# Kernel tuning notes

Measured on AMD Instinct MI355X. Metric: run time of the kernel, lower is better.

Reference implementation:

```python
import jax, jax.numpy as jnp
import numpy as np


def group_norm(x, g, b, groups, eps=1e-5):
    # x: (B, C, H, W), PyTorch GroupNorm semantics
    B, C, H, W = x.shape
    xr = x.reshape(B, groups, -1)
    m = xr.mean(-1, keepdims=True)
    v = xr.var(-1, keepdims=True)
    xn = ((xr - m) * jax.lax.rsqrt(v + eps)).reshape(B, C, H, W)
    return xn * g[:, None, None] + b[:, None, None]


def mamba(xs, in_w, conv_w, conv_b, xproj_w, dt_w, dt_b, A_log, D, out_w):
    # Standard Mamba block: in_proj -> causal depthwise conv -> SiLU ->
    # x_proj -> softplus(dt_proj) -> selective scan -> gate -> out_proj.
    Bsz, L, d = xs.shape
    di = in_w.shape[0] // 2
    r = dt_w.shape[1]
    n = A_log.shape[1]
    K = conv_w.shape[1]
    xz = xs @ in_w.T                           # (B, L, 2*di)
    xpart, z = xz[..., :di], xz[..., di:]
    xp = jnp.pad(xpart, ((0, 0), (K - 1, 0), (0, 0)))  # causal pad
    xc = conv_b + sum(xp[:, k:k + L, :] * conv_w[:, k] for k in range(K))
    xc = jax.nn.silu(xc)
    proj = xc @ xproj_w.T                      # (B, L, r + 2n)
    dt = proj[..., :r]
    Bm = proj[..., r:r + n]
    Cm = proj[..., r + n:]
    delta = jax.nn.softplus(dt @ dt_w.T + dt_b)   # (B, L, di)
    A = -jnp.exp(A_log)                            # (di, n)
    dA = jnp.exp(jnp.einsum('bld,dn->bldn', delta, A))
    dBu = jnp.einsum('bld,bln,bld->bldn', delta, Bm, xc)

    def step(h, inp):
        dA_t, dBu_t, C_t = inp
        h = dA_t * h + dBu_t                  # (B, di, n)
        return h, jnp.einsum('bdn,bn->bd', h, C_t)

    h0 = jnp.zeros((Bsz, di, n), xs.dtype)
    _, ys = jax.lax.scan(step, h0, (jnp.moveaxis(dA, 1, 0), jnp.moveaxis(dBu, 1, 0), jnp.moveaxis(Cm, 1, 0)))
    y = jnp.moveaxis(ys, 0, 1) + D * xc
    y = y * jax.nn.silu(z)
    return y @ out_w.T


def setup_inputs() -> dict:
    def nrm(i, shape, s=0.05):
        return jax.random.normal(jax.random.fold_in(jax.random.key(0), i), shape, dtype=jnp.float32) * s

    f32 = jnp.float32
    C = 128
    di, r, n = 256, 8, 16          # spa mamba: d_model=128, expand=2
    di2, r2 = 64, 2                # spe mamba: d_model=32
    A1 = jnp.log(jnp.broadcast_to(jnp.arange(1, n + 1, dtype=f32), (di, n)))
    A2 = jnp.log(jnp.broadcast_to(jnp.arange(1, n + 1, dtype=f32), (di2, n)))
    return {
        'x': nrm(0, (2, C, 64, 64), 1.0),
        'pe_w': nrm(1, (C, C)), 'pe_b': jnp.zeros((C,), f32),
        'pe_gn_g': jnp.ones((C,), f32), 'pe_gn_b': jnp.zeros((C,), f32),
        'spa_in_w': nrm(2, (2 * di, C)),
        'spa_conv_w': nrm(3, (di, 4)), 'spa_conv_b': jnp.zeros((di,), f32),
        'spa_xproj_w': nrm(4, (r + 2 * n, di)),
        'spa_dt_w': nrm(5, (di, r)), 'spa_dt_b': jnp.full((di,), -2.0, f32),
        'spa_Alog': A1, 'spa_D': jnp.ones((di,), f32),
        'spa_out_w': nrm(6, (C, di)),
        'spa_gn_g': jnp.ones((C,), f32), 'spa_gn_b': jnp.zeros((C,), f32),
        'spe_in_w': nrm(7, (2 * di2, 32)),
        'spe_conv_w': nrm(8, (di2, 4)), 'spe_conv_b': jnp.zeros((di2,), f32),
        'spe_xproj_w': nrm(9, (r2 + 2 * n, di2)),
        'spe_dt_w': nrm(10, (di2, r2)), 'spe_dt_b': jnp.full((di2,), -2.0, f32),
        'spe_Alog': A2, 'spe_D': jnp.ones((di2,), f32),
        'spe_out_w': nrm(11, (32, di2)),
        'spe_gn_g': jnp.ones((C,), f32), 'spe_gn_b': jnp.zeros((C,), f32),
        'fuse_w': jnp.full((2,), 0.5, f32),
        'cls_w': nrm(12, (10, C)), 'cls_b': jnp.zeros((10,), f32),
        'ref_dw_w': nrm(13, (C, 1, 3, 3)),
        'ref_gn_g': jnp.ones((C,), f32), 'ref_gn_b': jnp.zeros((C,), f32),
        'ref_pw_w': nrm(14, (1, C)), 'ref_pw_b': jnp.zeros((1,), f32),
        'alpha': jnp.asarray(1e-4, f32),
    }


def reference(x, pe_w, pe_b, pe_gn_g, pe_gn_b, spa_in_w, spa_conv_w, spa_conv_b, spa_xproj_w, spa_dt_w, spa_dt_b, spa_Alog, spa_D, spa_out_w, spa_gn_g, spa_gn_b, spe_in_w, spe_conv_w, spe_conv_b, spe_xproj_w, spe_dt_w, spe_dt_b, spe_Alog, spe_D, spe_out_w, spe_gn_g, spe_gn_b, fuse_w, cls_w, cls_b, ref_dw_w, ref_gn_g, ref_gn_b, ref_pw_w, ref_pw_b, alpha):
    B, _, H, W = x.shape
    # patch embedding: 1x1 conv + GroupNorm + SiLU
    h1 = jnp.einsum('bchw,oc->bohw', x, pe_w) + pe_b[:, None, None]
    h1 = jax.nn.silu(group_norm(h1, pe_gn_g, pe_gn_b, 4))
    # SpaMamba: scan over flattened spatial tokens (B, H*W, C)
    seq = h1.transpose(0, 2, 3, 1).reshape(B, H * W, -1)
    y = mamba(seq, spa_in_w, spa_conv_w, spa_conv_b, spa_xproj_w, spa_dt_w, spa_dt_b, spa_Alog, spa_D, spa_out_w)
    y = y.reshape(B, H, W, -1).transpose(0, 3, 1, 2)
    spa = jax.nn.silu(group_norm(y, spa_gn_g, spa_gn_b, 4)) + h1
    # SpeMamba: token_num=4, group_channel_num=32, channel_num=128 (no pad)
    seq2 = h1.transpose(0, 2, 3, 1).reshape(B * H * W, 4, 32)
    y2 = mamba(seq2, spe_in_w, spe_conv_w, spe_conv_b, spe_xproj_w, spe_dt_w, spe_dt_b, spe_Alog, spe_D, spe_out_w)
    y2 = y2.reshape(B, H, W, -1).transpose(0, 3, 1, 2)
    spe = h1 + jax.nn.silu(group_norm(y2, spe_gn_g, spe_gn_b, 4))
    # attention-weighted fusion + residual (BothMamba, use_att=True)
    wts = jax.nn.softmax(fuse_w)
    feat = spa * wts[0] + spe * wts[1] + h1
    # classifier head (1x1 conv)
    logits = jnp.einsum('bchw,oc->bohw', feat, cls_w) + cls_b[:, None, None]
    # BoundaryAwareLogitRefiner
    edge = jax.lax.conv_general_dilated(feat, ref_dw_w, (1, 1), ((1, 1), (1, 1)), feature_group_count=feat.shape[1], dimension_numbers=('NCHW', 'OIHW', 'NCHW'))
    edge = jax.nn.silu(group_norm(edge, ref_gn_g, ref_gn_b, 4))
    edge = jax.nn.sigmoid(jnp.einsum('bchw,oc->bohw', edge, ref_pw_w) + ref_pw_b[:, None, None])
    local = jax.lax.reduce_window(logits, 0.0, jax.lax.add, (1, 1, 3, 3), (1, 1, 1, 1), ((0, 0), (0, 0), (1, 1), (1, 1))) / 9.0  # count_include_pad=True
    return logits + alpha * (1.0 - edge) * (local - logits)
```

## Files before the change

### kernel.cpp

```cpp
#include <hip/hip_runtime.h>
#include <math.h>

#define DEV __device__ __forceinline__

DEV float sigm(float x){ return 1.f/(1.f+__expf(-x)); }
DEV float siluf(float x){ return x * sigm(x); }
DEV float softplusf(float x){ return x > 20.f ? x : log1pf(__expf(x)); }

static constexpr float NG = 131072.0f;
static constexpr float LOG2E = 1.4426950408889634f;

static constexpr size_t WS_H1    = 0;
static constexpr size_t WS_H1PRE = 1048576;
static constexpr size_t WS_XC    = 2097152;
static constexpr size_t WS_ZSIL  = 4194304;
static constexpr size_t WS_XZD   = 6291456;
static constexpr size_t WS_QOFF  = 8388608;
static constexpr size_t WS_LOG   = 8650752;
static constexpr size_t WS_Y     = 10485760;
static constexpr size_t WS_POFF  = 12582912;
static constexpr size_t WS_Y2    = 14155776;
static constexpr size_t WS_PROJ  = 15204352;

DEV void reduce_part(const float* __restrict__ part, int rowsPerB, float* dst16){
  int tid = threadIdx.x;
  int p = tid >> 4, sl = tid & 15;
  int b = p >> 3, j = p & 7;
  float s = 0.f;
  for (int row = sl; row < rowsPerB; row += 16)
    s += part[((size_t)b*rowsPerB + row)*8 + j];
  s += __shfl_xor(s,1); s += __shfl_xor(s,2);
  s += __shfl_xor(s,4); s += __shfl_xor(s,8);
  if (sl == 0) dst16[p] = s;
  __syncthreads();
}

__global__ void __launch_bounds__(256)
k_pe(const float* __restrict__ x, const float* __restrict__ pe_w,
     const float* __restrict__ pe_b, float* __restrict__ h1pre,
     float* __restrict__ part){
  __shared__ float As[16][36];
  __shared__ float Bs[16][64];
  __shared__ float red1[2][4], red2[2][4];
  int tid = threadIdx.x;
  int nx = blockIdx.x, my = blockIdx.y;
  int m0 = my*32, n0 = nx*64;
  int b = m0 >> 12, pl0 = m0 & 4095;
  int tx = tid & 15, ty = tid >> 4;
  float acc[2][4];
  #pragma unroll
  for (int i = 0; i < 2; i++)
    #pragma unroll
    for (int j = 0; j < 4; j++) acc[i][j] = 0.f;
  for (int k0 = 0; k0 < 128; k0 += 16){
    if (tid < 128){
      int k = tid >> 3, mm = (tid & 7)*4;
      float4 a = *(const float4*)(x + ((size_t)b*128 + k0+k)*4096 + pl0 + mm);
      *(float4*)&As[k][mm] = a;
    }
    {
      int n = tid >> 2, kq = (tid & 3)*4;
      float4 a = *(const float4*)(pe_w + (size_t)(n0+n)*128 + k0 + kq);
      Bs[kq+0][n] = a.x; Bs[kq+1][n] = a.y; Bs[kq+2][n] = a.z; Bs[kq+3][n] = a.w;
    }
    __syncthreads();
    #pragma unroll
    for (int k = 0; k < 16; k++){
      float2 av = *(const float2*)&As[k][ty*2];
      float4 bv = *(const float4*)&Bs[k][tx*4];
      acc[0][0] += av.x*bv.x; acc[0][1] += av.x*bv.y; acc[0][2] += av.x*bv.z; acc[0][3] += av.x*bv.w;
      acc[1][0] += av.y*bv.x; acc[1][1] += av.y*bv.y; acc[1][2] += av.y*bv.z; acc[1][3] += av.y*bv.w;
    }
    __syncthreads();
  }
  float4 bias = *(const float4*)(pe_b + n0 + tx*4);
  float s1 = 0.f, s2 = 0.f;
  #pragma unroll
  for (int i = 0; i < 2; i++){
    float4 st;
    st.x = acc[i][0]+bias.x; st.y = acc[i][1]+bias.y;
    st.z = acc[i][2]+bias.z; st.w = acc[i][3]+bias.w;
    s1 += st.x+st.y+st.z+st.w;
    s2 += st.x*st.x + st.y*st.y + st.z*st.z + st.w*st.w;
    *(float4*)(h1pre + (size_t)(m0 + ty*2 + i)*128 + n0 + tx*4) = st;
  }
  s1 += __shfl_xor(s1,1);  s2 += __shfl_xor(s2,1);
  s1 += __shfl_xor(s1,2);  s2 += __shfl_xor(s2,2);
  s1 += __shfl_xor(s1,4);  s2 += __shfl_xor(s2,4);
  s1 += __shfl_xor(s1,16); s2 += __shfl_xor(s2,16);
  s1 += __shfl_xor(s1,32); s2 += __shfl_xor(s2,32);
  int lane = tid & 63, w = tid >> 6;
  if ((lane & 55) == 0){
    int gl = (lane >> 3) & 1;
    red1[gl][w] = s1; red2[gl][w] = s2;
  }
  __syncthreads();
  if (tid < 8){
    int gg = tid >> 1, which = tid & 1;
    int gl = gg - nx*2;
    float v = 0.f;
    if (gl == 0 || gl == 1){
      v = which ? (red2[gl][0]+red2[gl][1]+red2[gl][2]+red2[gl][3])
                : (red1[gl][0]+red1[gl][1]+red1[gl][2]+red1[gl][3]);
    }
    int pblk = b*256 + (my & 127)*2 + nx;
    part[(size_t)pblk*8 + tid] = v;
  }
}

__global__ void __launch_bounds__(256)
k_xz(const float* __restrict__ h1pre, const float* __restrict__ in_w,
     const float* __restrict__ partPE, const float* __restrict__ gng,
     const float* __restrict__ gnb, float* __restrict__ h1,
     float* __restrict__ xzd, float* __restrict__ zsil){
  __shared__ float As[16][68];
  __shared__ float Bs[16][64];
  __shared__ float sst[16];
  reduce_part(partPE, 256, sst);
  int tid = threadIdx.x;
  int m0 = blockIdx.y*64, n0 = blockIdx.x*64;
  int tx = tid & 15, ty = tid >> 4;
  float acc[4][4];
  #pragma unroll
  for (int i = 0; i < 4; i++)
    #pragma unroll
    for (int j = 0; j < 4; j++) acc[i][j] = 0.f;
  for (int k0 = 0; k0 < 128; k0 += 16){
    {
      int m = tid >> 2, kk = (tid & 3)*4;
      int pixm = m0 + m, c0 = k0 + kk;
      int bb = pixm >> 12, g = c0 >> 5;
      float4 a = *(const float4*)(h1pre + (size_t)pixm*128 + c0);
      float mu = sst[bb*8 + g*2] * (1.f/NG);
      float var = sst[bb*8 + g*2 + 1] * (1.f/NG) - mu*mu;
      float rs = rsqrtf(var + 1e-5f);
      float4 gg = *(const float4*)(gng + c0);
      float4 gb = *(const float4*)(gnb + c0);
      float4 v;
      v.x = siluf((a.x-mu)*rs*gg.x + gb.x);
      v.y = siluf((a.y-mu)*rs*gg.y + gb.y);
      v.z = siluf((a.z-mu)*rs*gg.z + gb.z);
      v.w = siluf((a.w-mu)*rs*gg.w + gb.w);
      As[kk+0][m] = v.x; As[kk+1][m] = v.y; As[kk+2][m] = v.z; As[kk+3][m] = v.w;
      if (blockIdx.x == 0) *(float4*)(h1 + (size_t)pixm*128 + c0) = v;
    }
    {
      int n = tid >> 2, kq = (tid & 3)*4;
      float4 a = *(const float4*)(in_w + (size_t)(n0+n)*128 + k0 + kq);
      Bs[kq+0][n] = a.x; Bs[kq+1][n] = a.y; Bs[kq+2][n] = a.z; Bs[kq+3][n] = a.w;
    }
    __syncthreads();
    #pragma unroll
    for (int k = 0; k < 16; k++){
      float4 av = *(const float4*)&As[k][ty*4];
      float4 bv = *(const float4*)&Bs[k][tx*4];
      acc[0][0] += av.x*bv.x; acc[0][1] += av.x*bv.y; acc[0][2] += av.x*bv.z; acc[0][3] += av.x*bv.w;
      acc[1][0] += av.y*bv.x; acc[1][1] += av.y*bv.y; acc[1][2] += av.y*bv.z; acc[1][3] += av.y*bv.w;
      acc[2][0] += av.z*bv.x; acc[2][1] += av.z*bv.y; acc[2][2] += av.z*bv.z; acc[2][3] += av.z*bv.w;
      acc[3][0] += av.w*bv.x; acc[3][1] += av.w*bv.y; acc[3][2] += av.w*bv.z; acc[3][3] += av.w*bv.w;
    }
    __syncthreads();
  }
  if (n0 < 256){
    #pragma unroll
    for (int i = 0; i < 4; i++){
      float4 st; st.x = acc[i][0]; st.y = acc[i][1]; st.z = acc[i][2]; st.w = acc[i][3];
      *(float4*)(xzd + (size_t)(m0 + ty*4 + i)*256 + n0 + tx*4) = st;
    }
  } else {
    #pragma unroll
    for (int i = 0; i < 4; i++){
      float4 st;
      st.x = siluf(acc[i][0]); st.y = siluf(acc[i][1]);
      st.z = siluf(acc[i][2]); st.w = siluf(acc[i][3]);
      *(float4*)(zsil + (size_t)(m0 + ty*4 + i)*256 + (n0-256) + tx*4) = st;
    }
  }
}

__global__ void __launch_bounds__(256)
k_projc(const float* __restrict__ xzd, const float* __restrict__ cw,
        const float* __restrict__ cb, const float* __restrict__ xpw,
        const float* __restrict__ dtw, const float* __restrict__ dtb,
        const float* __restrict__ Alog,
        float* __restrict__ xc, float* __restrict__ proj,
        float* __restrict__ delta, float* __restrict__ P,
        float* __restrict__ Q){
  __shared__ float xct[16*260];
  __shared__ float s_pr[16][40];
  int tid = threadIdx.x;
  int bc = blockIdx.x;
  int m0 = bc * 16;
  {
    int slot = tid >> 6, lane = tid & 63;
    int d4 = lane*4;
    float4 cbv = *(const float4*)(cb + d4);
    float4 cw0 = *(const float4*)(cw + (size_t)(d4+0)*4);
    float4 cw1 = *(const float4*)(cw + (size_t)(d4+1)*4);
    float4 cw2 = *(const float4*)(cw + (size_t)(d4+2)*4);
    float4 cw3 = *(const float4*)(cw + (size_t)(d4+3)*4);
    const float* c0p = (const float*)&cw0;
    const float* c1p = (const float*)&cw1;
    const float* c2p = (const float*)&cw2;
    const float* c3p = (const float*)&cw3;
    for (int i = 0; i < 4; i++){
      int t = slot*4 + i;
      int tok = m0 + t;
      int l = tok & 4095;
      float4 acc = cbv;
      #pragma unroll
      for (int k = 0; k < 4; k++){
        int ls = l - 3 + k;
        if (ls >= 0){
          float4 xv = *(const float4*)(xzd + (size_t)(tok-3+k)*256 + d4);
          acc.x += xv.x * c0p[k];
          acc.y += xv.y * c1p[k];
          acc.z += xv.z * c2p[k];
          acc.w += xv.w * c3p[k];
        }
      }
      float4 s;
      s.x = siluf(acc.x); s.y = siluf(acc.y); s.z = siluf(acc.z); s.w = siluf(acc.w);
      *(float4*)&xct[t*260 + d4] = s;
      *(float4*)(xc + (size_t)tok*256 + d4) = s;
    }
  }
  __syncthreads();
  {
    int t = tid & 15, jq = tid >> 4;
    int tok = m0 + t;
    float a0 = 0.f, a1 = 0.f, a2 = 0.f;
    for (int k0 = 0; k0 < 256; k0 += 4){
      float4 av = *(const float4*)&xct[t*260 + k0];
      float4 w0 = *(const float4*)(xpw + (size_t)jq*256 + k0);
      float4 w1 = *(const float4*)(xpw + (size_t)(jq+16)*256 + k0);
      a0 += av.x*w0.x + av.y*w0.y + av.z*w0.z + av.w*w0.w;
      a1 += av.x*w1.x + av.y*w1.y + av.z*w1.z + av.w*w1.w;
      if (jq < 8){
        float4 w2 = *(const float4*)(xpw + (size_t)(jq+32)*256 + k0);
        a2 += av.x*w2.x + av.y*w2.y + av.z*w2.z + av.w*w2.w;
      }
    }
    float* pr = proj + (size_t)tok*40;
    pr[jq] = a0;      s_pr[t][jq] = a0;
    pr[jq+16] = a1;   s_pr[t][jq+16] = a1;
    if (jq < 8){ pr[jq+32] = a2; s_pr[t][jq+32] = a2; }
  }
  __syncthreads();
  {
    int d = tid;
    const float4* wr = (const float4*)(dtw + (size_t)d*8);
    float4 w0 = wr[0], w1 = wr[1];
    float bd = dtb[d];
    float An[16];
    {
      const float4* ar = (const float4*)(Alog + (size_t)d*16);
      #pragma unroll
      for (int k = 0; k < 4; k++){
        float4 a = ar[k];
        An[k*4]   = -__expf(a.x)*LOG2E; An[k*4+1] = -__expf(a.y)*LOG2E;
        An[k*4+2] = -__expf(a.z)*LOG2E; An[k*4+3] = -__expf(a.w)*LOG2E;
      }
    }
    float Pv[16], Qv[16];
    #pragma unroll
    for (int n = 0; n < 16; n++){ Pv[n] = 1.f; Qv[n] = 0.f; }
    for (int t = 0; t < 16; t++){
      float dv = bd + s_pr[t][0]*w0.x + s_pr[t][1]*w0.y + s_pr[t][2]*w0.z + s_pr[t][3]*w0.w
                    + s_pr[t][4]*w1.x + s_pr[t][5]*w1.y + s_pr[t][6]*w1.z + s_pr[t][7]*w1.w;
      dv = softplusf(dv);
      delta[(size_t)(m0+t)*256 + d] = dv;
      float xv = xct[t*260 + d];
      float dBx = dv*xv;
      #pragma unroll
      for (int n = 0; n < 16; n++){
        float a = exp2f(dv*An[n]);
        Qv[n] = a*Qv[n] + s_pr[t][8+n]*dBx;
        Pv[n] *= a;
      }
    }
    float* Pp = P + (size_t)bc*4096 + d*16;
    float* Qp = Q + (size_t)bc*4096 + d*16;
    #pragma unroll
    for (int k = 0; k < 4; k++){
      float4 pv; pv.x=Pv[k*4]; pv.y=Pv[k*4+1]; pv.z=Pv[k*4+2]; pv.w=Pv[k*4+3];
      float4 qv; qv.x=Qv[k*4]; qv.y=Qv[k*4+1]; qv.z=Qv[k*4+2]; qv.w=Qv[k*4+3];
      *(float4*)(Pp + k*4) = pv;
      *(float4*)(Qp + k*4) = qv;
    }
  }
}

__global__ void __launch_bounds__(256)
k_scan2(const float* __restrict__ P, const float* __restrict__ Q,
        float* __restrict__ hs){
  __shared__ float Ps[256][17], Qs[256][17];
  int tid = threadIdx.x;
  int b = blockIdx.x >> 8;
  int dn0 = (blockIdx.x & 255) * 16;
  for (int i = tid; i < 1024; i += 256){
    int ch = i >> 2, g = (i & 3)*4;
    size_t gaddr = (size_t)(b*256+ch)*4096 + dn0 + g;
    float4 p = *(const float4*)(P + gaddr);
    float4 q = *(const float4*)(Q + gaddr);
    Ps[ch][g]=p.x; Ps[ch][g+1]=p.y; Ps[ch][g+2]=p.z; Ps[ch][g+3]=p.w;
    Qs[ch][g]=q.x; Qs[ch][g+1]=q.y; Qs[ch][g+2]=q.z; Qs[ch][g+3]=q.w;
  }
  __syncthreads();
  int lane = tid & 63, wv = tid >> 6;
  for (int rep = 0; rep < 4; rep++){
    int c = wv*4 + rep;
    float p0 = Ps[4*lane+0][c], q0 = Qs[4*lane+0][c];
    float p1 = Ps[4*lane+1][c], q1 = Qs[4*lane+1][c];
    float p2 = Ps[4*lane+2][c], q2 = Qs[4*lane+2][c];
    float p3 = Ps[4*lane+3][c], q3 = Qs[4*lane+3][c];
    float p = p0, q = q0;
    q = p1*q + q1; p *= p1;
    q = p2*q + q2; p *= p2;
    q = p3*q + q3; p *= p3;
    #pragma unroll
    for (int off = 1; off < 64; off <<= 1){
      float pp = __shfl_up(p, off);
      float qp = __shfl_up(q, off);
      if (lane >= off){ q = p*qp + q; p = p*pp; }
    }
    float h0 = __shfl_up(q, 1);
    if (lane == 0) h0 = 0.f;
    float h1 = p0*h0 + q0;
    float h2 = p1*h1 + q1;
    float h3 = p2*h2 + q2;
    Ps[4*lane+0][c] = h0;
    Ps[4*lane+1][c] = h1;
    Ps[4*lane+2][c] = h2;
    Ps[4*lane+3][c] = h3;
  }
  __syncthreads();
  for (int i = tid; i < 1024; i += 256){
    int ch = i >> 2, g = (i & 3)*4;
    size_t gaddr = (size_t)(b*256+ch)*4096 + dn0 + g;
    float4 h;
    h.x = Ps[ch][g]; h.y = Ps[ch][g+1]; h.z = Ps[ch][g+2]; h.w = Ps[ch][g+3];
    *(float4*)(hs + gaddr) = h;
  }
}

__global__ void __launch_bounds__(256)
k_scan3(const float* __restrict__ delta, const float* __restrict__ proj,
        const float* __restrict__ xc, const float* __restrict__ zsil,
        const float* __restrict__ Alog, const float* __restrict__ Dv,
        const float* __restrict__ hs, float* __restrict__ y){
  int blk = blockIdx.x;
  int dblk = blk & 3;
  int bc = blk >> 2;
  int b = bc >> 8, chunk = bc & 255;
  int tid = threadIdx.x;
  int dl = tid >> 2, ng = tid & 3;
  int d = dblk*64 + dl;
  float4 a4 = *(const float4*)(Alog + (size_t)d*16 + ng*4);
  float An[4] = {-__expf(a4.x)*LOG2E, -__expf(a4.y)*LOG2E,
                 -__expf(a4.z)*LOG2E, -__expf(a4.w)*LOG2E};
  float Dd = Dv[d];
  float h[4];
  {
    size_t o = (size_t)bc*4096 + dblk*1024 + tid*4;
    float4 hv = *(const float4*)(hs + o);
    h[0]=hv.x; h[1]=hv.y; h[2]=hv.z; h[3]=hv.w;
  }
  size_t row0 = (size_t)(b*4096 + chunk*16);
  for (int l = 0; l < 16; l++){
    size_t r = row0 + l;
    float dv = delta[r*256 + d];
    float xv = xc[r*256 + d];
    float4 bm = *(const float4*)(proj + r*40 + 8 + ng*4);
    float4 cm = *(const float4*)(proj + r*40 + 24 + ng*4);
    float dBx = dv*xv;
    float bmv[4] = {bm.x, bm.y, bm.z, bm.w};
    float cmv[4] = {cm.x, cm.y, cm.z, cm.w};
    float ys = 0.f;
    #pragma unroll
    for (int k = 0; k < 4; k++){
      float a = exp2f(dv*An[k]);
      h[k] = a*h[k] + bmv[k]*dBx;
      ys += h[k]*cmv[k];
    }
    ys += __shfl_xor(ys, 1);
    ys += __shfl_xor(ys, 2);
    if (ng == 0){
      float zv = zsil[r*256 + d];
      y[r*256 + d] = (ys + Dd*xv) * zv;
    }
  }
}

__global__ void __launch_bounds__(256)
k_outproj(const float* __restrict__ y, const float* __restrict__ out_w,
          float* __restrict__ yproj, float* __restrict__ part){
  __shared__ float As[16][36];
  __shared__ float Bs[16][64];
  __shared__ float red1[2][4], red2[2][4];
  int tid = threadIdx.x;
  int nx = blockIdx.x, my = blockIdx.y;
  int m0 = my*32, n0 = nx*64;
  int b = m0 >> 12;
  int tx = tid & 15, ty = tid >> 4;
  float acc[2][4];
  #pragma unroll
  for (int i = 0; i < 2; i++)
    #pragma unroll
    for (int j = 0; j < 4; j++) acc[i][j] = 0.f;
  for (int k0 = 0; k0 < 256; k0 += 16){
    if (tid < 128){
      int m = tid >> 2, kk = (tid & 3)*4;
      float4 a = *(const float4*)(y + (size_t)(m0+m)*256 + k0+kk);
      As[kk+0][m] = a.x; As[kk+1][m] = a.y; As[kk+2][m] = a.z; As[kk+3][m] = a.w;
    }
    {
      int n = tid >> 2, kq = (tid & 3)*4;
      float4 a = *(const float4*)(out_w + (size_t)(n0+n)*256 + k0 + kq);
      Bs[kq+0][n] = a.x; Bs[kq+1][n] = a.y; Bs[kq+2][n] = a.z; Bs[kq+3][n] = a.w;
    }
    __syncthreads();
    #pragma unroll
    for (int k = 0; k < 16; k++){
      float2 av = *(const float2*)&As[k][ty*2];
      float4 bv = *(const float4*)&Bs[k][tx*4];
      acc[0][0] += av.x*bv.x; acc[0][1] += av.x*bv.y; acc[0][2] += av.x*bv.z; acc[0][3] += av.x*bv.w;
      acc[1][0] += av.y*bv.x; acc[1][1] += av.y*bv.y; acc[1][2] += av.y*bv.z; acc[1][3] += av.y*bv.w;
    }
    __syncthreads();
  }
  float s1 = 0.f, s2 = 0.f;
  #pragma unroll
  for (int i = 0; i < 2; i++){
    float4 st; st.x = acc[i][0]; st.y = acc[i][1]; st.z = acc[i][2]; st.w = acc[i][3];
    s1 += st.x+st.y+st.z+st.w;
    s2 += st.x*st.x + st.y*st.y + st.z*st.z + st.w*st.w;
    *(float4*)(yproj + (size_t)(m0 + ty*2 + i)*128 + n0 + tx*4) = st;
  }
  s1 += __shfl_xor(s1,1);  s2 += __shfl_xor(s2,1);
  s1 += __shfl_xor(s1,2);  s2 += __shfl_xor(s2,2);
  s1 += __shfl_xor(s1,4);  s2 += __shfl_xor(s2,4);
  s1 += __shfl_xor(s1,16); s2 += __shfl_xor(s2,16);
  s1 += __shfl_xor(s1,32); s2 += __shfl_xor(s2,32);
  int lane = tid & 63, w = tid >> 6;
  if ((lane & 55) == 0){
    int gl = (lane >> 3) & 1;
    red1[gl][w] = s1; red2[gl][w] = s2;
  }
  __syncthreads();
  if (tid < 8){
    int gg = tid >> 1, which = tid & 1;
    int gl = gg - nx*2;
    float v = 0.f;
    if (gl == 0 || gl == 1){
      v = which ? (red2[gl][0]+red2[gl][1]+red2[gl][2]+red2[gl][3])
                : (red1[gl][0]+red1[gl][1]+red1[gl][2]+red1[gl][3]);
    }
    int pblk = b*256 + (my & 127)*2 + nx;
    part[(size_t)pblk*8 + tid] = v;
  }
}

__global__ void __launch_bounds__(256)
k_spe_ab(const float* __restrict__ h1, const float* __restrict__ in_w,
         const float* __restrict__ conv_w, const float* __restrict__ conv_b,
         const float* __restrict__ xpw, float* __restrict__ xc2,
         float* __restrict__ zsil2, float* __restrict__ proj2){
  __shared__ float s_in[4][128];
  __shared__ float s_xc[64][66];
  int tid = threadIdx.x;
  int w = tid >> 6, lane = tid & 63;
  {
    float wx[32], wz[32];
    const float4* rx = (const float4*)(in_w + (size_t)lane*32);
    const float4* rz = (const float4*)(in_w + (size_t)(64+lane)*32);
    #pragma unroll
    for (int k = 0; k < 8; k++){
      float4 a = rx[k]; wx[k*4]=a.x; wx[k*4+1]=a.y; wx[k*4+2]=a.z; wx[k*4+3]=a.w;
      float4 b = rz[k]; wz[k*4]=b.x; wz[k*4+1]=b.y; wz[k*4+2]=b.z; wz[k*4+3]=b.w;
    }
    float4 cwv = ((const float4*)conv_w)[lane];
    float cbv = conv_b[lane];
    for (int i = 0; i < 4; i++){
      int pix = blockIdx.x*16 + w*4 + i;
      float2 hv = ((const float2*)(h1 + (size_t)pix*128))[lane];
      s_in[w][2*lane] = hv.x; s_in[w][2*lane+1] = hv.y;
      float xpr[4], zs[4];
      #pragma unroll
      for (int l = 0; l < 4; l++){
        const float4* sv = (const float4*)&s_in[w][l*32];
        float ax = 0.f, az = 0.f;
        #pragma unroll
        for (int c4 = 0; c4 < 8; c4++){
          float4 v = sv[c4];
          ax += v.x*wx[c4*4] + v.y*wx[c4*4+1] + v.z*wx[c4*4+2] + v.w*wx[c4*4+3];
          az += v.x*wz[c4*4] + v.y*wz[c4*4+1] + v.z*wz[c4*4+2] + v.w*wz[c4*4+3];
        }
        xpr[l] = ax; zs[l] = siluf(az);
      }
      #pragma unroll
      for (int l = 0; l < 4; l++){
        float v = cbv;
        if (l >= 3) v += xpr[l-3]*cwv.x;
        if (l >= 2) v += xpr[l-2]*cwv.y;
        if (l >= 1) v += xpr[l-1]*cwv.z;
        v += xpr[l]*cwv.w;
        float sx = siluf(v);
        int t = (w*4+i)*4 + l;
        int tok = blockIdx.x*64 + t;
        s_xc[t][lane] = sx;
        xc2 [(size_t)tok*64 + lane] = sx;
        zsil2[(size_t)tok*64 + lane] = zs[l];
      }
    }
  }
  __syncthreads();
  {
    int t = lane;
    float a[9];
    #pragma unroll
    for (int j = 0; j < 9; j++) a[j] = 0.f;
    for (int k = 0; k < 64; k++){
      float xk = s_xc[t][k];
      #pragma unroll
      for (int j = 0; j < 9; j++){
        int ja = w*9 + j; if (ja > 33) ja = 33;
        a[j] += xk * xpw[(size_t)ja*64 + k];
      }
    }
    float* pr = proj2 + (size_t)(blockIdx.x*64 + t)*36;
    #pragma unroll
    for (int j = 0; j < 9; j++){
      int ja = w*9 + j;
      if (ja < 34) pr[ja] = a[j];
    }
  }
}

__global__ void __launch_bounds__(256)
k_spe_cd(const float* __restrict__ xc2, const float* __restrict__ zsil2,
         const float* __restrict__ proj, const float* __restrict__ dt_w,
         const float* __restrict__ dt_b, const float* __restrict__ Alog,
         const float* __restrict__ Dvec, const float* __restrict__ out_w,
         float* __restrict__ y2, float* __restrict__ part){
  __shared__ float s_y[64][68];
  __shared__ float ldsWT[64*32];
  __shared__ float bst[8];
  int tid = threadIdx.x;
  int w = tid >> 6, lane = tid & 63;
  for (int i = tid; i < 2048; i += 256){
    int c2 = i >> 6, dd = i & 63;
    ldsWT[dd*32 + c2] = out_w[i];
  }
  if (tid < 8) bst[tid] = 0.f;
  {
    float2 dtwv = ((const float2*)dt_w)[lane];
    float dbv = dt_b[lane], Dd = Dvec[lane];
    float An[16];
    const float4* ar = (const float4*)(Alog + (size_t)lane*16);
    #pragma unroll
    for (int k = 0; k < 4; k++){
      float4 a = ar[k];
      An[k*4]   = -__expf(a.x)*LOG2E; An[k*4+1] = -__expf(a.y)*LOG2E;
      An[k*4+2] = -__expf(a.z)*LOG2E; An[k*4+3] = -__expf(a.w)*LOG2E;
    }
    for (int i = 0; i < 4; i++){
      int pix = blockIdx.x*16 + w*4 + i;
      float h[16];
      #pragma unroll
      for (int n = 0; n < 16; n++) h[n] = 0.f;
      #pragma unroll
      for (int l = 0; l < 4; l++){
        int tok = pix*4 + l;
        float pj[36];
        {
          const float4* pr = (const float4*)(proj + (size_t)tok*36);
          #pragma unroll
          for (int k = 0; k < 9; k++){
            float4 v = pr[k];
            pj[k*4]=v.x; pj[k*4+1]=v.y; pj[k*4+2]=v.z; pj[k*4+3]=v.w;
          }
        }
        float xv = xc2[(size_t)tok*64 + lane];
        float zv = zsil2[(size_t)tok*64 + lane];
        float dt = softplusf(dbv + pj[0]*dtwv.x + pj[1]*dtwv.y);
        float ys = 0.f;
        #pragma unroll
        for (int n = 0; n < 16; n++){
          float a = exp2f(dt * An[n]);
          h[n] = a*h[n] + dt * pj[2+n] * xv;
          ys += h[n] * pj[18+n];
        }
        s_y[(w*4+i)*4 + l][lane] = (ys + Dd*xv) * zv;
      }
    }
  }
  __syncthreads();
  {
    int c2 = lane & 31, slot = lane >> 5;
    int tl0 = w*16 + slot;
    float acc[8];
    #pragma unroll
    for (int i = 0; i < 8; i++) acc[i] = 0.f;
    for (int dd4 = 0; dd4 < 16; dd4++){
      float w0 = ldsWT[(dd4*4+0)*32 + c2];
      float w1 = ldsWT[(dd4*4+1)*32 + c2];
      float w2 = ldsWT[(dd4*4+2)*32 + c2];
      float w3 = ldsWT[(dd4*4+3)*32 + c2];
      #pragma unroll
      for (int i = 0; i < 8; i++){
        int t = tl0 + 2*i;
        float4 yv = *(const float4*)&s_y[t][dd4*4];
        acc[i] += yv.x*w0 + yv.y*w1 + yv.z*w2 + yv.w*w3;
      }
    }
    #pragma unroll
    for (int i = 0; i < 8; i++){
      int tok = blockIdx.x*64 + tl0 + 2*i;
      int pix = tok >> 2, l = tok & 3;
      y2[(size_t)pix*128 + l*32 + c2] = acc[i];
      float s1 = acc[i], s2 = acc[i]*acc[i];
      s1 += __shfl_xor(s1,1);  s2 += __shfl_xor(s2,1);
      s1 += __shfl_xor(s1,2);  s2 += __shfl_xor(s2,2);
      s1 += __shfl_xor(s1,4);  s2 += __shfl_xor(s2,4);
      s1 += __shfl_xor(s1,8);  s2 += __shfl_xor(s2,8);
      s1 += __shfl_xor(s1,16); s2 += __shfl_xor(s2,16);
      if (c2 == 0){
        atomicAdd(&bst[l*2+0], s1);
        atomicAdd(&bst[l*2+1], s2);
      }
    }
  }
  __syncthreads();
  if (tid < 8) part[(size_t)blockIdx.x*8 + tid] = bst[tid];
}

__global__ void __launch_bounds__(256)
k_fusedw(const float* __restrict__ h1, const float* __restrict__ yproj,
         const float* __restrict__ y2, const float* __restrict__ partSPA,
         const float* __restrict__ partSPE,
         const float* __restrict__ spa_g, const float* __restrict__ spa_b,
         const float* __restrict__ spe_g, const float* __restrict__ spe_b,
         const float* __restrict__ fuse_w, const float* __restrict__ cls_w,
         const float* __restrict__ cls_b, const float* __restrict__ dww,
         float* __restrict__ logits, float* __restrict__ epre,
         float* __restrict__ part){
  __shared__ float ft[60*129];
  __shared__ float clsL[10*129];
  __shared__ float sst[32];
  __shared__ float red1[4][64], red2[4][64];
  int tid = threadIdx.x;
  reduce_part(partSPA, 256, sst);
  reduce_part(partSPE, 256, sst+16);
  for (int i = tid; i < 1280; i += 256){
    int o = i >> 7, cc = i & 127;
    clsL[o*129 + cc] = cls_w[o*128 + cc];
  }
  int blk = blockIdx.x;
  int b = blk >> 7, rem = blk & 127;
  int ty = rem >> 3, tx = rem & 7;
  int r0 = ty*4, c0 = tx*8;
  float e0 = __expf(fuse_w[0]), e1 = __expf(fuse_w[1]);
  float wA = e0/(e0+e1), wB = e1/(e0+e1);
  for (int idx = tid; idx < 7680; idx += 256){
    int pos = idx >> 7, c = idx & 127;
    int hr = pos/10, hc = pos - hr*10;
    int ry = r0 + hr - 1, rx = c0 + hc - 1;
    float f = 0.f;
    if (ry >= 0 && ry < 64 && rx >= 0 && rx < 64){
      size_t pix = (size_t)((b<<12)|(ry<<6)|rx);
      int g = c >> 5;
      float m1 = sst[b*8 + g*2]      * (1.f/NG);
      float v1 = sst[b*8 + g*2 + 1]  * (1.f/NG) - m1*m1;
      float m2 = sst[16 + b*8 + g*2] * (1.f/NG);
      float v2 = sst[16 + b*8 + g*2+1]*(1.f/NG) - m2*m2;
      float h = h1[pix*128 + c];
      float sa = siluf((yproj[pix*128+c]-m1)*rsqrtf(v1+1e-5f)*spa_g[c] + spa_b[c]) + h;
      float sp = h + siluf((y2[pix*128+c]-m2)*rsqrtf(v2+1e-5f)*spe_g[c] + spe_b[c]);
      f = sa*wA + sp*wB + h;
    }
    ft[pos*129 + c] = f;
  }
  __syncthreads();
  int c = tid & 127, pl = tid >> 7;
  float w9[9];
  #pragma unroll
  for (int k = 0; k < 9; k++) w9[k] = dww[c*9+k];
  float s1 = 0.f, s2 = 0.f;
  for (int i = 0; i < 16; i++){
    int px = i*2 + pl;
    int py = px >> 3, pxx = px & 7;
    float acc = 0.f;
    #pragma unroll
    for (int dy = 0; dy < 3; dy++)
      #pragma unroll
      for (int dx = 0; dx < 3; dx++)
        acc += ft[((py+dy)*10 + (pxx+dx))*129 + c] * w9[dy*3+dx];
    epre[(size_t)((b<<12)|((r0+py)<<6)|(c0+pxx))*128 + c] = acc;
    s1 += acc; s2 += acc*acc;
  }
  for (int idx = tid; idx < 320; idx += 256){
    int px = idx/10, o = idx - px*10;
    int py = px >> 3, pxx = px & 7;
    int pos = (py+1)*10 + (pxx+1);
    float acc = cls_b[o];
    for (int cc = 0; cc < 128; cc++)
      acc += ft[pos*129 + cc] * clsL[o*129 + cc];
    logits[(size_t)((b<<12)|((r0+py)<<6)|(c0+pxx))*16 + o] = acc;
  }
  int g = c >> 5;
  int ridx0 = (c & 31) | (pl << 5);
  red1[g][ridx0] = s1; red2[g][ridx0] = s2;
  __syncthreads();
  int rg = tid >> 6, ridx = tid & 63;
  for (int s = 32; s >= 1; s >>= 1){
    if (ridx < s){ red1[rg][ridx] += red1[rg][ridx+s]; red2[rg][ridx] += red2[rg][ridx+s]; }
    __syncthreads();
  }
  if (ridx == 0){
    part[(size_t)blk*8 + rg*2+0] = red1[rg][0];
    part[(size_t)blk*8 + rg*2+1] = red2[rg][0];
  }
}

__global__ void __launch_bounds__(256)
k_final(const float* __restrict__ epre, const float* __restrict__ logits,
        const float* __restrict__ partDW, const float* __restrict__ rg_g,
        const float* __restrict__ rg_b, const float* __restrict__ pw_w,
        const float* __restrict__ pw_b, const float* __restrict__ alpha,
        float* __restrict__ outp){
  __shared__ float sst[16];
  __shared__ float part[4];
  __shared__ float edge_s[2];
  reduce_part(partDW, 128, sst);
  int tid = threadIdx.x;
  int pixl = tid >> 7, c = tid & 127;
  int pix = blockIdx.x*2 + pixl;
  int b = pix >> 12, p = pix & 4095, yy = p >> 6, xx = p & 63;
  int g = c >> 5;
  float m = sst[b*8 + g*2]   * (1.f/NG);
  float v = sst[b*8 + g*2+1] * (1.f/NG) - m*m;
  float e = epre[(size_t)pix*128+c];
  float en = siluf((e-m)*rsqrtf(v+1e-5f)*rg_g[c] + rg_b[c]);
  float pv = en * pw_w[c];
  pv += __shfl_xor(pv,1);  pv += __shfl_xor(pv,2);  pv += __shfl_xor(pv,4);
  pv += __shfl_xor(pv,8);  pv += __shfl_xor(pv,16); pv += __shfl_xor(pv,32);
  if ((tid & 63) == 0) part[tid>>6] = pv;
  __syncthreads();
  if (tid < 2) edge_s[tid] = sigm(part[tid*2] + part[tid*2+1] + pw_b[0]);
  __syncthreads();
  if (c < 10){
    float ed = edge_s[pixl];
    int o = c;
    float lg = logits[(size_t)pix*16 + o];
    float loc = 0.f;
    for (int dy = -1; dy <= 1; dy++){
      int ny = yy+dy; if (ny < 0 || ny > 63) continue;
      for (int dx = -1; dx <= 1; dx++){
        int nx = xx+dx; if (nx < 0 || nx > 63) continue;
        loc += logits[(size_t)((b<<12)|(ny<<6)|nx)*16 + o];
      }
    }
    loc *= (1.f/9.f);
    outp[(size_t)((b*10+o)<<12) + p] = lg + alpha[0]*(1.f-ed)*(loc - lg);
  }
}

extern "C" void kernel_launch(void* const* d_in, const int* in_sizes, int n_in,
                              void* d_out, int out_size, void* d_ws, size_t ws_size,
                              hipStream_t stream){
  const float* x          = (const float*)d_in[0];
  const float* pe_w       = (const float*)d_in[1];
  const float* pe_b       = (const float*)d_in[2];
  const float* pe_gn_g    = (const float*)d_in[3];
  const float* pe_gn_b    = (const float*)d_in[4];
  const float* spa_in_w   = (const float*)d_in[5];
  const float* spa_conv_w = (const float*)d_in[6];
  const float* spa_conv_b = (const float*)d_in[7];
  const float* spa_xproj_w= (const float*)d_in[8];
  const float* spa_dt_w   = (const float*)d_in[9];
  const float* spa_dt_b   = (const float*)d_in[10];
  const float* spa_Alog   = (const float*)d_in[11];
  const float* spa_D      = (const float*)d_in[12];
  const float* spa_out_w  = (const float*)d_in[13];
  const float* spa_gn_g   = (const float*)d_in[14];
  const float* spa_gn_b   = (const float*)d_in[15];
  const float* spe_in_w   = (const float*)d_in[16];
  const float* spe_conv_w = (const float*)d_in[17];
  const float* spe_conv_b = (const float*)d_in[18];
  const float* spe_xproj_w= (const float*)d_in[19];
  const float* spe_dt_w   = (const float*)d_in[20];
  const float* spe_dt_b   = (const float*)d_in[21];
  const float* spe_Alog   = (const float*)d_in[22];
  const float* spe_D      = (const float*)d_in[23];
  const float* spe_out_w  = (const float*)d_in[24];
  const float* spe_gn_g   = (const float*)d_in[25];
  const float* spe_gn_b   = (const float*)d_in[26];
  const float* fuse_w     = (const float*)d_in[27];
  const float* cls_w      = (const float*)d_in[28];
  const float* cls_b      = (const float*)d_in[29];
  const float* ref_dw_w   = (const float*)d_in[30];
  const float* ref_gn_g   = (const float*)d_in[31];
  const float* ref_gn_b   = (const float*)d_in[32];
  const float* ref_pw_w   = (const float*)d_in[33];
  const float* ref_pw_b   = (const float*)d_in[34];
  const float* alpha      = (const float*)d_in[35];
  float* ws  = (float*)d_ws;
  float* out = (float*)d_out;

  float* Pb    = ws + WS_POFF;
  float* Qb    = ws + WS_QOFF;
  float* HSb   = Pb;
  float* dely  = ws + WS_Y;
  float* partPE  = ws + WS_Y;
  float* partSPA = ws + WS_POFF;
  float* partSPE = ws + WS_POFF + 16384;
  float* partDW  = ws + WS_POFF + 65536;
  float* proj  = ws + WS_PROJ;
  float* xc2   = ws + WS_XC;
  float* zsil2 = ws + WS_XZD;
  float* proj2 = ws + WS_QOFF;
  float* epre  = ws + WS_Y;

  k_pe<<<dim3(2,256),256,0,stream>>>(x, pe_w, pe_b, ws+WS_H1PRE, partPE);
  k_xz<<<dim3(8,128),256,0,stream>>>(ws+WS_H1PRE, spa_in_w, partPE,
      pe_gn_g, pe_gn_b, ws+WS_H1, ws+WS_XZD, ws+WS_ZSIL);
  k_projc<<<512,256,0,stream>>>(ws+WS_XZD, spa_conv_w, spa_conv_b, spa_xproj_w,
      spa_dt_w, spa_dt_b, spa_Alog, ws+WS_XC, proj, dely, Pb, Qb);
  k_scan2<<<512,256,0,stream>>>(Pb, Qb, HSb);
  k_scan3<<<2048,256,0,stream>>>(dely, proj, ws+WS_XC, ws+WS_ZSIL,
      spa_Alog, spa_D, HSb, dely);
  k_outproj<<<dim3(2,256),256,0,stream>>>(dely, spa_out_w, ws+WS_H1PRE, partSPA);
  k_spe_ab<<<512,256,0,stream>>>(ws+WS_H1, spe_in_w, spe_conv_w, spe_conv_b,
      spe_xproj_w, xc2, zsil2, proj2);
  k_spe_cd<<<512,256,0,stream>>>(xc2, zsil2, proj2, spe_dt_w, spe_dt_b,
      spe_Alog, spe_D, spe_out_w, ws+WS_Y2, partSPE);
  k_fusedw<<<256,256,0,stream>>>(ws+WS_H1, ws+WS_H1PRE, ws+WS_Y2,
      partSPA, partSPE, spa_gn_g, spa_gn_b, spe_gn_g, spe_gn_b,
      fuse_w, cls_w, cls_b, ref_dw_w, ws+WS_LOG, epre, partDW);
  k_final<<<4096,256,0,stream>>>(epre, ws+WS_LOG, partDW,
      ref_gn_g, ref_gn_b, ref_pw_w, ref_pw_b, alpha, out);
  (void)in_sizes; (void)n_in; (void)out_size; (void)ws_size;
}
```

Measured before the change: 392.8 us.

## Split chunk-scan prefix out of projc into a separate wider-parallel kernel

The per-chunk P/Q scan summary, which used to run inside k_projc with each thread holding 16 states, moves to a new k_scan1 kernel. That kernel launches four times as many blocks, and each thread handles 4 states for one channel. The goal is to spread the exp2-heavy work over more threads, cut register pressure and raise occupancy in k_projc. The cost is an extra launch plus re-reading delta, xc and proj from global memory.

```diff
diff --git a/kernel.cpp b/kernel.cpp
--- a/kernel.cpp
+++ b/kernel.cpp
@@ -182,15 +182,12 @@
 k_projc(const float* __restrict__ xzd, const float* __restrict__ cw,
         const float* __restrict__ cb, const float* __restrict__ xpw,
         const float* __restrict__ dtw, const float* __restrict__ dtb,
-        const float* __restrict__ Alog,
         float* __restrict__ xc, float* __restrict__ proj,
-        float* __restrict__ delta, float* __restrict__ P,
-        float* __restrict__ Q){
+        float* __restrict__ delta){
   __shared__ float xct[16*260];
-  __shared__ float s_pr[16][40];
-  int tid = threadIdx.x;
-  int bc = blockIdx.x;
-  int m0 = bc * 16;
+  __shared__ float s_dt[16][9];
+  int tid = threadIdx.x;
+  int m0 = blockIdx.x * 16;
   {
     int slot = tid >> 6, lane = tid & 63;
     int d4 = lane*4;
@@ -242,9 +239,9 @@
       }
     }
     float* pr = proj + (size_t)tok*40;
-    pr[jq] = a0;      s_pr[t][jq] = a0;
-    pr[jq+16] = a1;   s_pr[t][jq+16] = a1;
-    if (jq < 8){ pr[jq+32] = a2; s_pr[t][jq+32] = a2; }
+    pr[jq] = a0;
+    pr[jq+16] = a1;
+    if (jq < 8){ pr[jq+32] = a2; s_dt[t][jq] = a0; }
   }
   __syncthreads();
   {
@@ -252,43 +249,49 @@
     const float4* wr = (const float4*)(dtw + (size_t)d*8);
     float4 w0 = wr[0], w1 = wr[1];
     float bd = dtb[d];
-    float An[16];
-    {
-      const float4* ar = (const float4*)(Alog + (size_t)d*16);
-      #pragma unroll
-      for (int k = 0; k < 4; k++){
-        float4 a = ar[k];
-        An[k*4]   = -__expf(a.x)*LOG2E; An[k*4+1] = -__expf(a.y)*LOG2E;
-        An[k*4+2] = -__expf(a.z)*LOG2E; An[k*4+3] = -__expf(a.w)*LOG2E;
-      }
-    }
-    float Pv[16], Qv[16];
-    #pragma unroll
-    for (int n = 0; n < 16; n++){ Pv[n] = 1.f; Qv[n] = 0.f; }
     for (int t = 0; t < 16; t++){
-      float dv = bd + s_pr[t][0]*w0.x + s_pr[t][1]*w0.y + s_pr[t][2]*w0.z + s_pr[t][3]*w0.w
-                    + s_pr[t][4]*w1.x + s_pr[t][5]*w1.y + s_pr[t][6]*w1.z + s_pr[t][7]*w1.w;
-      dv = softplusf(dv);
-      delta[(size_t)(m0+t)*256 + d] = dv;
-      float xv = xct[t*260 + d];
-      float dBx = dv*xv;
-      #pragma unroll
-      for (int n = 0; n < 16; n++){
-        float a = exp2f(dv*An[n]);
-        Qv[n] = a*Qv[n] + s_pr[t][8+n]*dBx;
-        Pv[n] *= a;
-      }
-    }
-    float* Pp = P + (size_t)bc*4096 + d*16;
-    float* Qp = Q + (size_t)bc*4096 + d*16;
+      float v = bd + s_dt[t][0]*w0.x + s_dt[t][1]*w0.y + s_dt[t][2]*w0.z + s_dt[t][3]*w0.w
+                   + s_dt[t][4]*w1.x + s_dt[t][5]*w1.y + s_dt[t][6]*w1.z + s_dt[t][7]*w1.w;
+      delta[(size_t)(m0+t)*256 + d] = softplusf(v);
+    }
+  }
+}
+
+__global__ void __launch_bounds__(256)
+k_scan1(const float* __restrict__ delta, const float* __restrict__ proj,
+        const float* __restrict__ xc, const float* __restrict__ Alog,
+        float* __restrict__ P, float* __restrict__ Q){
+  int blk = blockIdx.x;
+  int dblk = blk & 3;
+  int bc = blk >> 2;
+  int b = bc >> 8, chunk = bc & 255;
+  int tid = threadIdx.x;
+  int dl = tid >> 2, ng = tid & 3;
+  int d = dblk*64 + dl;
+  float4 a4 = *(const float4*)(Alog + (size_t)d*16 + ng*4);
+  float An[4] = {-__expf(a4.x)*LOG2E, -__expf(a4.y)*LOG2E,
+                 -__expf(a4.z)*LOG2E, -__expf(a4.w)*LOG2E};
+  float Pv[4] = {1.f,1.f,1.f,1.f}, Qv[4] = {0.f,0.f,0.f,0.f};
+  size_t row0 = (size_t)(b*4096 + chunk*16);
+  for (int l = 0; l < 16; l++){
+    size_t r = row0 + l;
+    float dv = delta[r*256 + d];
+    float xv = xc[r*256 + d];
+    float4 bm = *(const float4*)(proj + r*40 + 8 + ng*4);
+    float dBx = dv*xv;
+    float bmv[4] = {bm.x, bm.y, bm.z, bm.w};
     #pragma unroll
     for (int k = 0; k < 4; k++){
-      float4 pv; pv.x=Pv[k*4]; pv.y=Pv[k*4+1]; pv.z=Pv[k*4+2]; pv.w=Pv[k*4+3];
-      float4 qv; qv.x=Qv[k*4]; qv.y=Qv[k*4+1]; qv.z=Qv[k*4+2]; qv.w=Qv[k*4+3];
-      *(float4*)(Pp + k*4) = pv;
-      *(float4*)(Qp + k*4) = qv;
-    }
-  }
+      float a = exp2f(dv*An[k]);
+      Qv[k] = a*Qv[k] + bmv[k]*dBx;
+      Pv[k] *= a;
+    }
+  }
+  size_t o = (size_t)bc*4096 + dblk*1024 + tid*4;
+  float4 pv; pv.x=Pv[0]; pv.y=Pv[1]; pv.z=Pv[2]; pv.w=Pv[3];
+  float4 qv; qv.x=Qv[0]; qv.y=Qv[1]; qv.z=Qv[2]; qv.w=Qv[3];
+  *(float4*)(P + o) = pv;
+  *(float4*)(Q + o) = qv;
 }
 
 __global__ void __launch_bounds__(256)
@@ -826,7 +829,8 @@
   k_xz<<<dim3(8,128),256,0,stream>>>(ws+WS_H1PRE, spa_in_w, partPE,
       pe_gn_g, pe_gn_b, ws+WS_H1, ws+WS_XZD, ws+WS_ZSIL);
   k_projc<<<512,256,0,stream>>>(ws+WS_XZD, spa_conv_w, spa_conv_b, spa_xproj_w,
-      spa_dt_w, spa_dt_b, spa_Alog, ws+WS_XC, proj, dely, Pb, Qb);
+      spa_dt_w, spa_dt_b, ws+WS_XC, proj, dely);
+  k_scan1<<<2048,256,0,stream>>>(dely, proj, ws+WS_XC, spa_Alog, Pb, Qb);
   k_scan2<<<512,256,0,stream>>>(Pb, Qb, HSb);
   k_scan3<<<2048,256,0,stream>>>(dely, proj, ws+WS_XC, ws+WS_ZSIL,
       spa_Alog, spa_D, HSb, dely);
```

Measured after the change: 379.0 us. 1.04x faster.
